# Kernel optimization log

Hardware: AMD Instinct MI355X
Metric: run time of the kernel (lower is better)

The kernel has to match this reference:

```python
import jax, jax.numpy as jnp
import numpy as np

HIDDEN = 3072
HEADS = 32
HEAD_DIM = HIDDEN // HEADS  # 96


def setup_inputs() -> dict:
    key = jax.random.key(0)
    k1, k2, k3, k4 = jax.random.split(key, 4)
    B, S = 2, 2048
    x = jax.random.normal(k1, (B, S, HIDDEN), dtype=jnp.float32)
    # qkv_proj: Linear(hidden, 3*hidden, bias=False); torch weight is [out,in]
    w_qkv = jax.random.normal(k2, (3 * HIDDEN, HIDDEN), dtype=jnp.float32) * (HIDDEN ** -0.5)
    # o_proj: Linear(hidden, hidden) with bias
    w_o = jax.random.normal(k3, (HIDDEN, HIDDEN), dtype=jnp.float32) * (HIDDEN ** -0.5)
    b_o = jax.random.normal(k4, (HIDDEN,), dtype=jnp.float32) * 0.01
    return {"x": x, "w_qkv": w_qkv, "w_o": w_o, "b_o": b_o}


def reference(x, w_qkv, w_o, b_o):
    B, S, _ = x.shape
    qkv = jnp.einsum('bsh,oh->bso', x, w_qkv)  # [B,S,3*HIDDEN]
    q, k, v = jnp.split(qkv, 3, axis=-1)
    # [B,S,HIDDEN] -> [B,H,S,D]
    def split_heads(t):
        return t.reshape(B, S, HEADS, HEAD_DIM).transpose(0, 2, 1, 3)
    q, k, v = split_heads(q), split_heads(k), split_heads(v)
    scores = jnp.einsum('bhqd,bhkd->bhqk', q, k) / jnp.sqrt(jnp.float32(HEAD_DIM))
    attn = jax.nn.softmax(scores, axis=-1)
    out = jnp.einsum('bhqk,bhkd->bhqd', attn, v)  # [B,H,S,D]
    out = out.transpose(0, 2, 1, 3).reshape(B, S, HIDDEN)
    return jnp.einsum('bsh,oh->bso', out, w_o) + b_o
```

## Files before the change

kernel.cpp:

```cpp
#include <hip/hip_runtime.h>
#include <math.h>


typedef unsigned int u32;
typedef unsigned short u16;
typedef __attribute__((ext_vector_type(8))) short bf16x8;
typedef __attribute__((ext_vector_type(4))) float f32x4;

#define MFMA(a, b, c) __builtin_amdgcn_mfma_f32_16x16x32_bf16((a), (b), (c), 0, 0, 0)

#define GLDS16(g, l) __builtin_amdgcn_global_load_lds( \
    (const __attribute__((address_space(1))) u32*)(g), \
    (__attribute__((address_space(3))) u32*)(l), 16, 0, 0)

__device__ __forceinline__ u16 f2bf(float f) {
  u32 u = __builtin_bit_cast(u32, f);
  return (u16)((u + 0x7fffu + ((u >> 16) & 1u)) >> 16);
}
__device__ __forceinline__ float bf2f(u16 h) {
  u32 u = ((u32)h) << 16;
  return __builtin_bit_cast(float, u);
}
__device__ __forceinline__ void split2(float f, u16& h, u16& l) {
  h = f2bf(f);
  l = f2bf(f - bf2f(h));
}
__device__ __forceinline__ bf16x8 ld16(const u16* p) {
  return *reinterpret_cast<const bf16x8*>(p);
}

__global__ void split_kernel(const float* __restrict__ src, u16* __restrict__ hi,
                             u16* __restrict__ lo, long n) {
  long i = ((long)blockIdx.x * 256 + threadIdx.x) * 4;
  if (i >= n) return;
  const float4 v = *reinterpret_cast<const float4*>(src + i);
  ushort4 h, l;
  split2(v.x, h.x, l.x);
  split2(v.y, h.y, l.y);
  split2(v.z, h.z, l.z);
  split2(v.w, h.w, l.w);
  *reinterpret_cast<ushort4*>(hi + i) = h;
  *reinterpret_cast<ushort4*>(lo + i) = l;
}

template <int MODE>
__global__ __launch_bounds__(512, 2) void gemm192(
    const u16* __restrict__ Ah, const u16* __restrict__ Al,
    const u16* __restrict__ Bh, const u16* __restrict__ Bl,
    int M, int N,
    u16* __restrict__ Ch, u16* __restrict__ Cl,
    float* __restrict__ Cf, const float* __restrict__ bias) {
  constexpr int NT = 144;
  constexpr int BOFF = 256 * 64;
  __shared__ u16 lds[2][(256 + 192) * 64];
  const int tid = threadIdx.x;
  const int lane = tid & 63;
  const int w = tid >> 6;
  const int wr = w >> 2, wc = w & 3;
  const int lr = lane & 15, lg = lane >> 4;

  const int mt = M >> 8;
  const int nwg = gridDim.x;
  const int bid = blockIdx.x;
  const int wg = (bid & 7) * (nwg >> 3) + (bid >> 3);
  const int bm = wg % mt, bn = wg / mt;

  const int srow = lane >> 3;
  const int sgc = ((lane & 7) ^ srow) * 8;

  auto stA = [&](int buf, int kt, int j) {
    const int seg = kt / 48;
    const int ko = (kt - seg * 48) * 64;
    const u16* P = (seg < 2) ? Ah : Al;
    const int r = j * 64 + w * 8 + srow;
    GLDS16(P + (long)(bm * 256 + r) * 3072 + ko + sgc,
           &lds[buf][(j * 64 + w * 8) * 64]);
  };
  auto stB = [&](int buf, int kt, int j) {
    const int seg = kt / 48;
    const int ko = (kt - seg * 48) * 64;
    const u16* P = (seg == 1) ? Bl : Bh;
    const int r = j * 64 + w * 8 + srow;
    GLDS16(P + (long)(bn * 192 + r) * 3072 + ko + sgc,
           &lds[buf][BOFF + (j * 64 + w * 8) * 64]);
  };

  f32x4 acc[8][3];
#pragma unroll
  for (int m = 0; m < 8; ++m)
#pragma unroll
    for (int n = 0; n < 3; ++n)
#pragma unroll
      for (int j = 0; j < 4; ++j) acc[m][n][j] = 0.f;

  stA(0, 0, 0); stA(0, 0, 1); stA(0, 0, 2); stA(0, 0, 3);
  stB(0, 0, 0); stB(0, 0, 1); stB(0, 0, 2);
  asm volatile("s_waitcnt vmcnt(0)" ::: "memory");
  __builtin_amdgcn_s_barrier();

  const int aRow0 = wr * 128 + lr;
  const int bRow0 = wc * 48 + lr;
  const int c0 = (lg ^ (lr & 7)) * 8;

#define RD_A(dst, MQ, KH)                                                  \
  _Pragma("unroll") for (int m = 0; m < 4; ++m) dst[m] =                   \
      ld16(&LA[(aRow0 + (MQ)*64 + m * 16) * 64 + (c0 ^ ((KH)*32))]);
#define RD_B(dst, KH)                                                      \
  _Pragma("unroll") for (int n = 0; n < 3; ++n) dst[n] =                   \
      ld16(&LB[(bRow0 + n * 16) * 64 + (c0 ^ ((KH)*32))]);
#define DO_MFMA(a, b, MQ)                                                  \
  __builtin_amdgcn_s_setprio(1);                                           \
  _Pragma("unroll") for (int m = 0; m < 4; ++m)                            \
  _Pragma("unroll") for (int n = 0; n < 3; ++n)                            \
      acc[(MQ)*4 + m][n] = MFMA(a[m], b[n], acc[(MQ)*4 + m][n]);           \
  __builtin_amdgcn_s_setprio(0);
#define PH_SYNC()                                                          \
  __builtin_amdgcn_s_barrier();                                            \
  asm volatile("s_waitcnt lgkmcnt(0)" ::: "memory");                       \
  __builtin_amdgcn_sched_barrier(0);

  for (int t = 0; t < NT; ++t) {
    const int cur = t & 1;
    const int nxt = cur ^ 1;
    const bool hn = (t + 1 < NT);
    const u16* LA = &lds[cur][0];
    const u16* LB = &lds[cur][BOFF];
    bf16x8 a0[4], a1[4], bk0[3], bk1[3];
    RD_B(bk0, 0);
    RD_A(a0, 0, 0);
    if (hn) { stA(nxt, t + 1, 0); stA(nxt, t + 1, 1); }
    PH_SYNC();
    DO_MFMA(a0, bk0, 0);
    __builtin_amdgcn_s_barrier();
    RD_B(bk1, 1);
    RD_A(a0, 0, 1);
    if (hn) { stA(nxt, t + 1, 2); stA(nxt, t + 1, 3); }
    PH_SYNC();
    DO_MFMA(a0, bk1, 0);
    __builtin_amdgcn_s_barrier();
    RD_A(a1, 1, 0);
    if (hn) { stB(nxt, t + 1, 0); stB(nxt, t + 1, 1); stB(nxt, t + 1, 2); }
    PH_SYNC();
    DO_MFMA(a1, bk0, 1);
    __builtin_amdgcn_s_barrier();
    RD_A(a1, 1, 1);
    PH_SYNC();
    DO_MFMA(a1, bk1, 1);
    asm volatile("s_waitcnt vmcnt(0)" ::: "memory");
    __builtin_amdgcn_s_barrier();
  }
#undef RD_A
#undef RD_B
#undef DO_MFMA
#undef PH_SYNC

#pragma unroll
  for (int m = 0; m < 8; ++m)
#pragma unroll
    for (int j = 0; j < 4; ++j) {
      const long row = (long)bm * 256 + wr * 128 + m * 16 + lg * 4 + j;
#pragma unroll
      for (int n = 0; n < 3; ++n) {
        const long col = (long)bn * 192 + wc * 48 + n * 16 + lr;
        const long idx = row * N + col;
        const float v = acc[m][n][j];
        if (MODE == 0) {
          u16 h, l;
          split2(v, h, l);
          Ch[idx] = h;
          Cl[idx] = l;
        } else {
          Cf[idx] = v + bias[col];
        }
      }
    }
}

__global__ void pack_k(const u16* __restrict__ QKVh, const u16* __restrict__ QKVl,
                       u16* __restrict__ Kp) {
  const int t = blockIdx.x * 256 + threadIdx.x;
  const int lane = t & 63;
  const int rec3 = t >> 6;
  const int c = rec3 % 3;
  const int kb = (rec3 / 3) & 127;
  const int hl = rec3 / 384;
  const int lr = lane & 15, lg = lane >> 4;
  const long src =
      ((long)((hl >> 5) * 2048 + kb * 16 + lr)) * 9216 + 3072 + (hl & 31) * 96 + c * 32 + lg * 8;
  const long dst = ((long)rec3 * 2) * 512 + lane * 8;
  *reinterpret_cast<bf16x8*>(Kp + dst) = ld16(QKVh + src);
  *reinterpret_cast<bf16x8*>(Kp + dst + 512) = ld16(QKVl + src);
}

__global__ __launch_bounds__(256) void pack_v(const u16* __restrict__ QKVh,
                                              const u16* __restrict__ QKVl,
                                              u16* __restrict__ Vp) {
  __shared__ u16 sV[2][32 * 96];
  const int tid = threadIdx.x;
  const int hl = blockIdx.x >> 6;
  const int kq = blockIdx.x & 63;
  const long rowbase = ((long)((hl >> 5) * 2048 + kq * 32)) * 9216 + 6144 + (hl & 31) * 96;
#pragma unroll
  for (int i = 0; i < 3; ++i) {
    const int idx = i * 256 + tid;
    const int pl = idx / 384;
    const int r2 = idx % 384;
    const int row = r2 / 12, cu = r2 % 12;
    const u16* srcp = (pl ? QKVl : QKVh) + rowbase + (long)row * 9216 + cu * 8;
    *reinterpret_cast<bf16x8*>(&sV[pl][row * 96 + cu * 8]) = ld16(srcp);
  }
  __syncthreads();
#pragma unroll
  for (int i = 0; i < 3; ++i) {
    const int idx = i * 256 + tid;
    const int lane = idx & 63;
    const int rl = idx >> 6;
    const int n = rl >> 1, pl = rl & 1;
    const int lr = lane & 15, lg = lane >> 4;
    bf16x8 o;
#pragma unroll
    for (int e = 0; e < 8; ++e) o[e] = (short)sV[pl][(lg * 8 + e) * 96 + n * 16 + lr];
    const long dst = ((((long)hl * 6 + n) * 64 + kq) * 2 + pl) * 512 + lane * 8;
    *reinterpret_cast<bf16x8*>(Vp + dst) = o;
  }
}

__global__ __launch_bounds__(256, 2) void attn_kernel(
    const u16* __restrict__ QKVh, const u16* __restrict__ QKVl,
    const u16* __restrict__ Kp, const u16* __restrict__ Vp,
    u16* __restrict__ AOh, u16* __restrict__ AOl) {
  __shared__ u16 kv[2][24 * 512];
  __shared__ u16 pb[4][2][512];
  const int lane = threadIdx.x & 63;
  const int wv = threadIdx.x >> 6;
  const int lr = lane & 15, lg = lane >> 4;

  const int nwg = gridDim.x;
  const int bid = blockIdx.x;
  const int wg = (bid & 7) * (nwg >> 3) + (bid >> 3);
  const int hl = wg >> 5;
  const int qblk = wg & 31;
  const int b = hl >> 5;
  const int q0 = qblk * 64 + wv * 16;

  bf16x8 qh[3], ql[3];
  {
    const long qofs = ((long)(b * 2048 + q0 + lr)) * 9216 + (hl & 31) * 96 + lg * 8;
#pragma unroll
    for (int c = 0; c < 3; ++c) {
      qh[c] = ld16(QKVh + qofs + c * 32);
      ql[c] = ld16(QKVl + qofs + c * 32);
    }
  }

  f32x4 o_acc[6];
#pragma unroll
  for (int n = 0; n < 6; ++n)
#pragma unroll
    for (int j = 0; j < 4; ++j) o_acc[n][j] = 0.f;
  float lsum[4] = {0.f, 0.f, 0.f, 0.f};

  const float scale = 0.10206207261596577f;
  u16* pbh = pb[wv][0];
  u16* pbl = pb[wv][1];

  auto stage = [&](int nb, int it) {
    const long kbase = ((long)hl * 768 + (long)it * 12) * 512;
    const long vbase = ((long)hl * 768 + (long)it * 2) * 512;
#pragma unroll
    for (int j = 0; j < 6; ++j) {
      const int r = wv * 6 + j;
      const u16* src;
      if (r < 12) {
        const int tt = r / 6, rc = r % 6;
        src = Kp + kbase + ((long)(tt * 6 + rc)) * 512 + lane * 8;
      } else {
        const int r2 = r - 12;
        src = Vp + vbase + ((long)((r2 >> 1) * 128 + (r2 & 1))) * 512 + lane * 8;
      }
      GLDS16(src, &kv[nb][r * 512]);
    }
  };

  stage(0, 0);
  __syncthreads();

  for (int it = 0; it < 64; ++it) {
    const int nb = it & 1;
    if (it < 63) stage(nb ^ 1, it + 1);
    const u16* L = kv[nb];

    f32x4 s0, s1;
#pragma unroll
    for (int j = 0; j < 4; ++j) { s0[j] = 0.f; s1[j] = 0.f; }
#pragma unroll
    for (int c = 0; c < 3; ++c) {
      const bf16x8 kh0 = ld16(L + (c * 2 + 0) * 512 + lane * 8);
      const bf16x8 kl0 = ld16(L + (c * 2 + 1) * 512 + lane * 8);
      const bf16x8 kh1 = ld16(L + (6 + c * 2 + 0) * 512 + lane * 8);
      const bf16x8 kl1 = ld16(L + (6 + c * 2 + 1) * 512 + lane * 8);
      s0 = MFMA(qh[c], kh0, s0);
      s1 = MFMA(qh[c], kh1, s1);
      s0 = MFMA(qh[c], kl0, s0);
      s1 = MFMA(qh[c], kl1, s1);
      s0 = MFMA(ql[c], kh0, s0);
      s1 = MFMA(ql[c], kh1, s1);
    }

#pragma unroll
    for (int j = 0; j < 4; ++j) {
      const float p0 = __expf(fmaf(s0[j], scale, -12.f));
      const float p1 = __expf(fmaf(s1[j], scale, -12.f));
      lsum[j] += p0 + p1;
      const int r = lg * 4 + j;
      const int key = j ^ lg;
      u16 h, l;
      split2(p0, h, l);
      const int a0 = r * 32 + ((((lr >> 3) ^ key) & 3) << 3) + (lr & 7);
      pbh[a0] = h;
      pbl[a0] = l;
      split2(p1, h, l);
      const int a1 = r * 32 + ((((2 + (lr >> 3)) ^ key) & 3) << 3) + (lr & 7);
      pbh[a1] = h;
      pbl[a1] = l;
    }
    const int rkey = (lr & 3) ^ (lr >> 2);
    const int ra = lr * 32 + (((lg ^ rkey) & 3) << 3);
    const bf16x8 pah = ld16(&pbh[ra]);
    const bf16x8 pal = ld16(&pbl[ra]);

#pragma unroll
    for (int n = 0; n < 6; ++n) {
      const bf16x8 vh = ld16(L + (12 + n * 2 + 0) * 512 + lane * 8);
      const bf16x8 vl = ld16(L + (12 + n * 2 + 1) * 512 + lane * 8);
      o_acc[n] = MFMA(pah, vh, o_acc[n]);
      o_acc[n] = MFMA(pah, vl, o_acc[n]);
      o_acc[n] = MFMA(pal, vh, o_acc[n]);
    }
    __syncthreads();
  }

  float inv[4];
#pragma unroll
  for (int j = 0; j < 4; ++j) {
    float rs = lsum[j];
#pragma unroll
    for (int mk = 1; mk < 16; mk <<= 1) rs += __shfl_xor(rs, mk);
    inv[j] = 1.f / rs;
  }
#pragma unroll
  for (int n = 0; n < 6; ++n)
#pragma unroll
    for (int j = 0; j < 4; ++j) {
      const long row = (long)(b * 2048 + q0 + lg * 4 + j);
      const long col = (long)(hl & 31) * 96 + n * 16 + lr;
      u16 h, l;
      split2(o_acc[n][j] * inv[j], h, l);
      AOh[row * 3072 + col] = h;
      AOl[row * 3072 + col] = l;
    }
}

extern "C" void kernel_launch(void* const* d_in, const int* in_sizes, int n_in,
                              void* d_out, int out_size, void* d_ws, size_t ws_size,
                              hipStream_t stream) {
  const float* x = (const float*)d_in[0];
  const float* wqkv = (const float*)d_in[1];
  const float* wo = (const float*)d_in[2];
  const float* bo = (const float*)d_in[3];
  float* out = (float*)d_out;
  char* ws = (char*)d_ws;

  const size_t E_X = (size_t)4096 * 3072;
  const size_t E_WQ = (size_t)9216 * 3072;
  const size_t E_QKV = (size_t)4096 * 9216;

  u16* XH = (u16*)ws;
  u16* XL = XH + E_X;
  char* W0 = ws + 4 * E_X;
  u16* WQH = (u16*)W0;
  u16* WQL = WQH + E_WQ;
  char* Q0 = W0 + 4 * E_WQ;
  u16* QKVH = (u16*)Q0;
  u16* QKVL = QKVH + E_QKV;
  char* V0 = Q0 + 4 * E_QKV;
  u16* VP = (u16*)V0;
  u16* KP = (u16*)ws;
  u16* AOH = (u16*)W0;
  u16* AOL = AOH + E_X;
  u16* WOH = (u16*)(W0 + 4 * E_X);
  u16* WOL = WOH + (size_t)3072 * 3072;

  const size_t need = 4 * (E_X + E_WQ + E_QKV + E_X);
  if (ws_size < need) return;

  split_kernel<<<12288, 256, 0, stream>>>(x, XH, XL, (long)E_X);
  split_kernel<<<27648, 256, 0, stream>>>(wqkv, WQH, WQL, (long)E_WQ);
  gemm192<0><<<768, 512, 0, stream>>>(XH, XL, WQH, WQL, 4096, 9216,
                                      QKVH, QKVL, nullptr, nullptr);
  pack_k<<<6144, 256, 0, stream>>>(QKVH, QKVL, KP);
  pack_v<<<4096, 256, 0, stream>>>(QKVH, QKVL, VP);
  split_kernel<<<9216, 256, 0, stream>>>(wo, WOH, WOL, (long)(3072 * 3072));
  attn_kernel<<<2048, 256, 0, stream>>>(QKVH, QKVL, KP, VP, AOH, AOL);
  gemm192<1><<<256, 512, 0, stream>>>(AOH, AOL, WOH, WOL, 4096, 3072,
                                      nullptr, nullptr, out, bo);
}
```

Measured before the change: 1.375 ms.

## Triple-buffer A tiles with prefetch distance two and drop per-phase barriers

Splits the shared LDS tile into a triple-buffered A region and a double-buffered B region. A tiles are now prefetched two K-steps ahead, B tiles one step ahead, with partial vmcnt waits so loads stay in flight across iterations. The intra-iteration barrier plus lgkmcnt sync before each MFMA phase is removed, so ds_read ordering is left to the compiler. In exchange LDS use grows to about 144KB per block, and the synchronisation depends on careful vmcnt accounting.

```diff
diff --git a/kernel.cpp b/kernel.cpp
--- a/kernel.cpp
+++ b/kernel.cpp
@@ -51,8 +51,8 @@
     u16* __restrict__ Ch, u16* __restrict__ Cl,
     float* __restrict__ Cf, const float* __restrict__ bias) {
   constexpr int NT = 144;
-  constexpr int BOFF = 256 * 64;
-  __shared__ u16 lds[2][(256 + 192) * 64];
+  __shared__ u16 ldsA[3][256 * 64];
+  __shared__ u16 ldsB[2][192 * 64];
   const int tid = threadIdx.x;
   const int lane = tid & 63;
   const int w = tid >> 6;
@@ -74,7 +74,7 @@
     const u16* P = (seg < 2) ? Ah : Al;
     const int r = j * 64 + w * 8 + srow;
     GLDS16(P + (long)(bm * 256 + r) * 3072 + ko + sgc,
-           &lds[buf][(j * 64 + w * 8) * 64]);
+           &ldsA[buf][(j * 64 + w * 8) * 64]);
   };
   auto stB = [&](int buf, int kt, int j) {
     const int seg = kt / 48;
@@ -82,7 +82,7 @@
     const u16* P = (seg == 1) ? Bl : Bh;
     const int r = j * 64 + w * 8 + srow;
     GLDS16(P + (long)(bn * 192 + r) * 3072 + ko + sgc,
-           &lds[buf][BOFF + (j * 64 + w * 8) * 64]);
+           &ldsB[buf][(j * 64 + w * 8) * 64]);
   };
 
   f32x4 acc[8][3];
@@ -95,7 +95,8 @@
 
   stA(0, 0, 0); stA(0, 0, 1); stA(0, 0, 2); stA(0, 0, 3);
   stB(0, 0, 0); stB(0, 0, 1); stB(0, 0, 2);
-  asm volatile("s_waitcnt vmcnt(0)" ::: "memory");
+  stA(1, 1, 0); stA(1, 1, 1); stA(1, 1, 2); stA(1, 1, 3);
+  asm volatile("s_waitcnt vmcnt(4)" ::: "memory");
   __builtin_amdgcn_s_barrier();
 
   const int aRow0 = wr * 128 + lr;
@@ -114,45 +115,39 @@
   _Pragma("unroll") for (int n = 0; n < 3; ++n)                            \
       acc[(MQ)*4 + m][n] = MFMA(a[m], b[n], acc[(MQ)*4 + m][n]);           \
   __builtin_amdgcn_s_setprio(0);
-#define PH_SYNC()                                                          \
-  __builtin_amdgcn_s_barrier();                                            \
-  asm volatile("s_waitcnt lgkmcnt(0)" ::: "memory");                       \
-  __builtin_amdgcn_sched_barrier(0);
-
+
+  int curA = 0;
   for (int t = 0; t < NT; ++t) {
-    const int cur = t & 1;
-    const int nxt = cur ^ 1;
-    const bool hn = (t + 1 < NT);
-    const u16* LA = &lds[cur][0];
-    const u16* LB = &lds[cur][BOFF];
+    const u16* LA = ldsA[curA];
+    const u16* LB = ldsB[t & 1];
+    const int nA = (curA + 2 >= 3) ? curA - 1 : curA + 2;
     bf16x8 a0[4], a1[4], bk0[3], bk1[3];
     RD_B(bk0, 0);
     RD_A(a0, 0, 0);
-    if (hn) { stA(nxt, t + 1, 0); stA(nxt, t + 1, 1); }
-    PH_SYNC();
+    if (t + 1 < NT) { stB((t + 1) & 1, t + 1, 0); stB((t + 1) & 1, t + 1, 1); stB((t + 1) & 1, t + 1, 2); }
     DO_MFMA(a0, bk0, 0);
     __builtin_amdgcn_s_barrier();
     RD_B(bk1, 1);
     RD_A(a0, 0, 1);
-    if (hn) { stA(nxt, t + 1, 2); stA(nxt, t + 1, 3); }
-    PH_SYNC();
+    if (t + 2 < NT) { stA(nA, t + 2, 0); stA(nA, t + 2, 1); }
     DO_MFMA(a0, bk1, 0);
     __builtin_amdgcn_s_barrier();
     RD_A(a1, 1, 0);
-    if (hn) { stB(nxt, t + 1, 0); stB(nxt, t + 1, 1); stB(nxt, t + 1, 2); }
-    PH_SYNC();
+    if (t + 2 < NT) { stA(nA, t + 2, 2); stA(nA, t + 2, 3); }
     DO_MFMA(a1, bk0, 1);
     __builtin_amdgcn_s_barrier();
     RD_A(a1, 1, 1);
-    PH_SYNC();
     DO_MFMA(a1, bk1, 1);
-    asm volatile("s_waitcnt vmcnt(0)" ::: "memory");
+    if (t + 2 < NT)
+      asm volatile("s_waitcnt vmcnt(4)" ::: "memory");
+    else
+      asm volatile("s_waitcnt vmcnt(0)" ::: "memory");
     __builtin_amdgcn_s_barrier();
+    curA = (curA + 1 >= 3) ? 0 : curA + 1;
   }
 #undef RD_A
 #undef RD_B
 #undef DO_MFMA
-#undef PH_SYNC
 
 #pragma unroll
   for (int m = 0; m < 8; ++m)
```

After: 1.585 ms. +15.3%, slower.

## Interleave hi/lo bf16 halves per 32-column block and fuse split-GEMM passes

Applied to the files above, without the earlier changes.

Stores the high and low bf16 parts of every tensor interleaved in 64-element chunks (32 hi, 32 lo), so one 64-wide K tile holds both halves of 32 columns. The GEMM then issues all three bf16 product terms (hh, hl, lh) from a single staged tile, which cuts the K loop from 144 to 96 iterations and reuses each loaded A/B fragment three times. Each iteration now has two sync phases instead of four, and all tile loads are issued up front. Every producer and consumer (split, pack_k, pack_v, attention, epilogues) is rewritten to use the interleaved indexing, so a single addressing mistake anywhere would break correctness.

```diff
diff --git a/kernel.cpp b/kernel.cpp
--- a/kernel.cpp
+++ b/kernel.cpp
@@ -29,30 +29,32 @@
   return *reinterpret_cast<const bf16x8*>(p);
 }
 
-__global__ void split_kernel(const float* __restrict__ src, u16* __restrict__ hi,
-                             u16* __restrict__ lo, long n) {
+__global__ void split_kernel(const float* __restrict__ src, u16* __restrict__ dst,
+                             long n) {
   long i = ((long)blockIdx.x * 256 + threadIdx.x) * 4;
   if (i >= n) return;
   const float4 v = *reinterpret_cast<const float4*>(src + i);
+  const u32 i32 = (u32)i;
+  const u32 row = i32 / 3072u;
+  const u32 col = i32 - row * 3072u;
+  const long base = (long)row * 6144 + (col >> 5) * 64 + (col & 31);
   ushort4 h, l;
   split2(v.x, h.x, l.x);
   split2(v.y, h.y, l.y);
   split2(v.z, h.z, l.z);
   split2(v.w, h.w, l.w);
-  *reinterpret_cast<ushort4*>(hi + i) = h;
-  *reinterpret_cast<ushort4*>(lo + i) = l;
+  *reinterpret_cast<ushort4*>(dst + base) = h;
+  *reinterpret_cast<ushort4*>(dst + base + 32) = l;
 }
 
 template <int MODE>
-__global__ __launch_bounds__(512, 2) void gemm192(
-    const u16* __restrict__ Ah, const u16* __restrict__ Al,
-    const u16* __restrict__ Bh, const u16* __restrict__ Bl,
+__global__ __launch_bounds__(512, 2) void gemm3t(
+    const u16* __restrict__ A2, const u16* __restrict__ B2,
     int M, int N,
-    u16* __restrict__ Ch, u16* __restrict__ Cl,
-    float* __restrict__ Cf, const float* __restrict__ bias) {
-  constexpr int NT = 144;
-  constexpr int BOFF = 256 * 64;
-  __shared__ u16 lds[2][(256 + 192) * 64];
+    u16* __restrict__ C2, float* __restrict__ Cf, const float* __restrict__ bias) {
+  constexpr int NT = 96;
+  __shared__ u16 ldsA[2][256 * 64];
+  __shared__ u16 ldsB[2][192 * 64];
   const int tid = threadIdx.x;
   const int lane = tid & 63;
   const int w = tid >> 6;
@@ -69,20 +71,14 @@
   const int sgc = ((lane & 7) ^ srow) * 8;
 
   auto stA = [&](int buf, int kt, int j) {
-    const int seg = kt / 48;
-    const int ko = (kt - seg * 48) * 64;
-    const u16* P = (seg < 2) ? Ah : Al;
     const int r = j * 64 + w * 8 + srow;
-    GLDS16(P + (long)(bm * 256 + r) * 3072 + ko + sgc,
-           &lds[buf][(j * 64 + w * 8) * 64]);
+    GLDS16(A2 + (long)(bm * 256 + r) * 6144 + kt * 64 + sgc,
+           &ldsA[buf][(j * 64 + w * 8) * 64]);
   };
   auto stB = [&](int buf, int kt, int j) {
-    const int seg = kt / 48;
-    const int ko = (kt - seg * 48) * 64;
-    const u16* P = (seg == 1) ? Bl : Bh;
     const int r = j * 64 + w * 8 + srow;
-    GLDS16(P + (long)(bn * 192 + r) * 3072 + ko + sgc,
-           &lds[buf][BOFF + (j * 64 + w * 8) * 64]);
+    GLDS16(B2 + (long)(bn * 192 + r) * 6144 + kt * 64 + sgc,
+           &ldsB[buf][(j * 64 + w * 8) * 64]);
   };
 
   f32x4 acc[8][3];
@@ -102,17 +98,20 @@
   const int bRow0 = wc * 48 + lr;
   const int c0 = (lg ^ (lr & 7)) * 8;
 
-#define RD_A(dst, MQ, KH)                                                  \
-  _Pragma("unroll") for (int m = 0; m < 4; ++m) dst[m] =                   \
-      ld16(&LA[(aRow0 + (MQ)*64 + m * 16) * 64 + (c0 ^ ((KH)*32))]);
-#define RD_B(dst, KH)                                                      \
-  _Pragma("unroll") for (int n = 0; n < 3; ++n) dst[n] =                   \
-      ld16(&LB[(bRow0 + n * 16) * 64 + (c0 ^ ((KH)*32))]);
-#define DO_MFMA(a, b, MQ)                                                  \
+#define RD_A(MQ)                                                           \
+  _Pragma("unroll") for (int m = 0; m < 4; ++m) {                          \
+    const int off = (aRow0 + (MQ)*64 + m * 16) * 64 + c0;                  \
+    ah[m] = ld16(&LA[off]);                                                \
+    al[m] = ld16(&LA[off ^ 32]);                                           \
+  }
+#define DO_MFMA3(MQ)                                                       \
   __builtin_amdgcn_s_setprio(1);                                           \
   _Pragma("unroll") for (int m = 0; m < 4; ++m)                            \
-  _Pragma("unroll") for (int n = 0; n < 3; ++n)                            \
-      acc[(MQ)*4 + m][n] = MFMA(a[m], b[n], acc[(MQ)*4 + m][n]);           \
+  _Pragma("unroll") for (int n = 0; n < 3; ++n) {                          \
+    acc[(MQ)*4 + m][n] = MFMA(ah[m], bh[n], acc[(MQ)*4 + m][n]);           \
+    acc[(MQ)*4 + m][n] = MFMA(ah[m], bl[n], acc[(MQ)*4 + m][n]);           \
+    acc[(MQ)*4 + m][n] = MFMA(al[m], bh[n], acc[(MQ)*4 + m][n]);           \
+  }                                                                        \
   __builtin_amdgcn_s_setprio(0);
 #define PH_SYNC()                                                          \
   __builtin_amdgcn_s_barrier();                                            \
@@ -122,36 +121,32 @@
   for (int t = 0; t < NT; ++t) {
     const int cur = t & 1;
     const int nxt = cur ^ 1;
-    const bool hn = (t + 1 < NT);
-    const u16* LA = &lds[cur][0];
-    const u16* LB = &lds[cur][BOFF];
-    bf16x8 a0[4], a1[4], bk0[3], bk1[3];
-    RD_B(bk0, 0);
-    RD_A(a0, 0, 0);
-    if (hn) { stA(nxt, t + 1, 0); stA(nxt, t + 1, 1); }
+    const u16* LA = ldsA[cur];
+    const u16* LB = ldsB[cur];
+    bf16x8 ah[4], al[4], bh[3], bl[3];
+#pragma unroll
+    for (int n = 0; n < 3; ++n) {
+      const int off = (bRow0 + n * 16) * 64 + c0;
+      bh[n] = ld16(&LB[off]);
+      bl[n] = ld16(&LB[off ^ 32]);
+    }
+    RD_A(0);
+    if (t + 1 < NT) {
+      stA(nxt, t + 1, 0); stA(nxt, t + 1, 1);
+      stA(nxt, t + 1, 2); stA(nxt, t + 1, 3);
+      stB(nxt, t + 1, 0); stB(nxt, t + 1, 1); stB(nxt, t + 1, 2);
+    }
     PH_SYNC();
-    DO_MFMA(a0, bk0, 0);
+    DO_MFMA3(0);
     __builtin_amdgcn_s_barrier();
-    RD_B(bk1, 1);
-    RD_A(a0, 0, 1);
-    if (hn) { stA(nxt, t + 1, 2); stA(nxt, t + 1, 3); }
+    RD_A(1);
     PH_SYNC();
-    DO_MFMA(a0, bk1, 0);
-    __builtin_amdgcn_s_barrier();
-    RD_A(a1, 1, 0);
-    if (hn) { stB(nxt, t + 1, 0); stB(nxt, t + 1, 1); stB(nxt, t + 1, 2); }
-    PH_SYNC();
-    DO_MFMA(a1, bk0, 1);
-    __builtin_amdgcn_s_barrier();
-    RD_A(a1, 1, 1);
-    PH_SYNC();
-    DO_MFMA(a1, bk1, 1);
+    DO_MFMA3(1);
     asm volatile("s_waitcnt vmcnt(0)" ::: "memory");
     __builtin_amdgcn_s_barrier();
   }
 #undef RD_A
-#undef RD_B
-#undef DO_MFMA
+#undef DO_MFMA3
 #undef PH_SYNC
 
 #pragma unroll
@@ -161,23 +156,22 @@
       const long row = (long)bm * 256 + wr * 128 + m * 16 + lg * 4 + j;
 #pragma unroll
       for (int n = 0; n < 3; ++n) {
-        const long col = (long)bn * 192 + wc * 48 + n * 16 + lr;
-        const long idx = row * N + col;
+        const int col = bn * 192 + wc * 48 + n * 16 + lr;
         const float v = acc[m][n][j];
         if (MODE == 0) {
+          const long idx = row * (2L * N) + (col >> 5) * 64 + (col & 31);
           u16 h, l;
           split2(v, h, l);
-          Ch[idx] = h;
-          Cl[idx] = l;
+          C2[idx] = h;
+          C2[idx + 32] = l;
         } else {
-          Cf[idx] = v + bias[col];
+          Cf[row * N + col] = v + bias[col];
         }
       }
     }
 }
 
-__global__ void pack_k(const u16* __restrict__ QKVh, const u16* __restrict__ QKVl,
-                       u16* __restrict__ Kp) {
+__global__ void pack_k(const u16* __restrict__ QKV2, u16* __restrict__ Kp) {
   const int t = blockIdx.x * 256 + threadIdx.x;
   const int lane = t & 63;
   const int rec3 = t >> 6;
@@ -185,29 +179,29 @@
   const int kb = (rec3 / 3) & 127;
   const int hl = rec3 / 384;
   const int lr = lane & 15, lg = lane >> 4;
-  const long src =
-      ((long)((hl >> 5) * 2048 + kb * 16 + lr)) * 9216 + 3072 + (hl & 31) * 96 + c * 32 + lg * 8;
+  const long src = ((long)((hl >> 5) * 2048 + kb * 16 + lr)) * 18432 +
+                   (96 + (hl & 31) * 3 + c) * 64 + lg * 8;
   const long dst = ((long)rec3 * 2) * 512 + lane * 8;
-  *reinterpret_cast<bf16x8*>(Kp + dst) = ld16(QKVh + src);
-  *reinterpret_cast<bf16x8*>(Kp + dst + 512) = ld16(QKVl + src);
-}
-
-__global__ __launch_bounds__(256) void pack_v(const u16* __restrict__ QKVh,
-                                              const u16* __restrict__ QKVl,
+  *reinterpret_cast<bf16x8*>(Kp + dst) = ld16(QKV2 + src);
+  *reinterpret_cast<bf16x8*>(Kp + dst + 512) = ld16(QKV2 + src + 32);
+}
+
+__global__ __launch_bounds__(256) void pack_v(const u16* __restrict__ QKV2,
                                               u16* __restrict__ Vp) {
   __shared__ u16 sV[2][32 * 96];
   const int tid = threadIdx.x;
   const int hl = blockIdx.x >> 6;
   const int kq = blockIdx.x & 63;
-  const long rowbase = ((long)((hl >> 5) * 2048 + kq * 32)) * 9216 + 6144 + (hl & 31) * 96;
+  const long rowbase = ((long)((hl >> 5) * 2048 + kq * 32)) * 18432 +
+                       (192 + (hl & 31) * 3) * 64;
 #pragma unroll
   for (int i = 0; i < 3; ++i) {
     const int idx = i * 256 + tid;
     const int pl = idx / 384;
     const int r2 = idx % 384;
     const int row = r2 / 12, cu = r2 % 12;
-    const u16* srcp = (pl ? QKVl : QKVh) + rowbase + (long)row * 9216 + cu * 8;
-    *reinterpret_cast<bf16x8*>(&sV[pl][row * 96 + cu * 8]) = ld16(srcp);
+    const long src = rowbase + (long)row * 18432 + (cu >> 2) * 64 + (cu & 3) * 8 + pl * 32;
+    *reinterpret_cast<bf16x8*>(&sV[pl][row * 96 + cu * 8]) = ld16(QKV2 + src);
   }
   __syncthreads();
 #pragma unroll
@@ -226,9 +220,9 @@
 }
 
 __global__ __launch_bounds__(256, 2) void attn_kernel(
-    const u16* __restrict__ QKVh, const u16* __restrict__ QKVl,
+    const u16* __restrict__ QKV2,
     const u16* __restrict__ Kp, const u16* __restrict__ Vp,
-    u16* __restrict__ AOh, u16* __restrict__ AOl) {
+    u16* __restrict__ AO2) {
   __shared__ u16 kv[2][24 * 512];
   __shared__ u16 pb[4][2][512];
   const int lane = threadIdx.x & 63;
@@ -245,11 +239,12 @@
 
   bf16x8 qh[3], ql[3];
   {
-    const long qofs = ((long)(b * 2048 + q0 + lr)) * 9216 + (hl & 31) * 96 + lg * 8;
+    const long qofs =
+        ((long)(b * 2048 + q0 + lr)) * 18432 + ((hl & 31) * 3) * 64 + lg * 8;
 #pragma unroll
     for (int c = 0; c < 3; ++c) {
-      qh[c] = ld16(QKVh + qofs + c * 32);
-      ql[c] = ld16(QKVl + qofs + c * 32);
+      qh[c] = ld16(QKV2 + qofs + c * 64);
+      ql[c] = ld16(QKV2 + qofs + c * 64 + 32);
     }
   }
 
@@ -353,11 +348,12 @@
 #pragma unroll
     for (int j = 0; j < 4; ++j) {
       const long row = (long)(b * 2048 + q0 + lg * 4 + j);
-      const long col = (long)(hl & 31) * 96 + n * 16 + lr;
+      const long idx =
+          row * 6144 + ((hl & 31) * 3 + (n >> 1)) * 64 + (n & 1) * 16 + lr;
       u16 h, l;
       split2(o_acc[n][j] * inv[j], h, l);
-      AOh[row * 3072 + col] = h;
-      AOl[row * 3072 + col] = l;
+      AO2[idx] = h;
+      AO2[idx + 32] = l;
     }
 }
 
@@ -374,34 +370,28 @@
   const size_t E_X = (size_t)4096 * 3072;
   const size_t E_WQ = (size_t)9216 * 3072;
   const size_t E_QKV = (size_t)4096 * 9216;
-
-  u16* XH = (u16*)ws;
-  u16* XL = XH + E_X;
+  const size_t E_WO = (size_t)3072 * 3072;
+
+  u16* X2 = (u16*)ws;
   char* W0 = ws + 4 * E_X;
-  u16* WQH = (u16*)W0;
-  u16* WQL = WQH + E_WQ;
+  u16* W2 = (u16*)W0;
   char* Q0 = W0 + 4 * E_WQ;
-  u16* QKVH = (u16*)Q0;
-  u16* QKVL = QKVH + E_QKV;
+  u16* QKV2 = (u16*)Q0;
   char* V0 = Q0 + 4 * E_QKV;
   u16* VP = (u16*)V0;
   u16* KP = (u16*)ws;
-  u16* AOH = (u16*)W0;
-  u16* AOL = AOH + E_X;
-  u16* WOH = (u16*)(W0 + 4 * E_X);
-  u16* WOL = WOH + (size_t)3072 * 3072;
+  u16* AO2 = (u16*)W0;
+  u16* WO2 = (u16*)(W0 + 4 * E_X);
 
   const size_t need = 4 * (E_X + E_WQ + E_QKV + E_X);
   if (ws_size < need) return;
 
-  split_kernel<<<12288, 256, 0, stream>>>(x, XH, XL, (long)E_X);
-  split_kernel<<<27648, 256, 0, stream>>>(wqkv, WQH, WQL, (long)E_WQ);
-  gemm192<0><<<768, 512, 0, stream>>>(XH, XL, WQH, WQL, 4096, 9216,
-                                      QKVH, QKVL, nullptr, nullptr);
-  pack_k<<<6144, 256, 0, stream>>>(QKVH, QKVL, KP);
-  pack_v<<<4096, 256, 0, stream>>>(QKVH, QKVL, VP);
-  split_kernel<<<9216, 256, 0, stream>>>(wo, WOH, WOL, (long)(3072 * 3072));
-  attn_kernel<<<2048, 256, 0, stream>>>(QKVH, QKVL, KP, VP, AOH, AOL);
-  gemm192<1><<<256, 512, 0, stream>>>(AOH, AOL, WOH, WOL, 4096, 3072,
-                                      nullptr, nullptr, out, bo);
-}
+  split_kernel<<<12288, 256, 0, stream>>>(x, X2, (long)E_X);
+  split_kernel<<<27648, 256, 0, stream>>>(wqkv, W2, (long)E_WQ);
+  gemm3t<0><<<768, 512, 0, stream>>>(X2, W2, 4096, 9216, QKV2, nullptr, nullptr);
+  pack_k<<<6144, 256, 0, stream>>>(QKV2, KP);
+  pack_v<<<4096, 256, 0, stream>>>(QKV2, VP);
+  split_kernel<<<9216, 256, 0, stream>>>(wo, WO2, (long)E_WO);
+  attn_kernel<<<2048, 256, 0, stream>>>(QKV2, KP, VP, AO2);
+  gemm3t<1><<<256, 512, 0, stream>>>(AO2, WO2, 4096, 3072, nullptr, out, bo);
+}
```

New measurement: 1.303 ms. 5.2% less time.
